# Kernel optimization log

Hardware: AMD Instinct MI355X
Metric: run time of the kernel (lower is better)

## Reference

```python
import jax, jax.numpy as jnp
import numpy as np

B, N, D_IN, D_OUT, H = 1, 4096, 512, 512, 8
DH = D_OUT // H


def setup_inputs() -> dict:
    key = jax.random.key(0)
    ks = jax.random.split(key, 8)
    s_in = 1.0 / np.sqrt(D_IN)
    h = jax.random.normal(ks[0], (B, N, D_IN), dtype=jnp.float32)
    adj_matrix = jax.random.uniform(ks[1], (B, N, N), dtype=jnp.float32)
    mask_matrix = jnp.zeros((B, N, N), dtype=jnp.float32)
    Wq = jax.random.uniform(ks[2], (D_IN, D_OUT), minval=-s_in, maxval=s_in, dtype=jnp.float32)
    Wk = jax.random.uniform(ks[3], (D_IN, D_OUT), minval=-s_in, maxval=s_in, dtype=jnp.float32)
    Wv = jax.random.uniform(ks[4], (D_IN, D_OUT), minval=-s_in, maxval=s_in, dtype=jnp.float32)
    bq = jax.random.uniform(ks[5], (D_OUT,), minval=-s_in, maxval=s_in, dtype=jnp.float32)
    bk = jax.random.uniform(ks[6], (D_OUT,), minval=-s_in, maxval=s_in, dtype=jnp.float32)
    bv = jax.random.uniform(ks[7], (D_OUT,), minval=-s_in, maxval=s_in, dtype=jnp.float32)
    return {"h": h, "adj_matrix": adj_matrix, "mask_matrix": mask_matrix,
            "Wq": Wq, "bq": bq, "Wk": Wk, "bk": bk, "Wv": Wv, "bv": bv}


def reference(h, adj_matrix, mask_matrix, Wq, bq, Wk, bk, Wv, bv):
    # Q/K/V projections: (B, N, D_OUT)
    Q = h @ Wq + bq
    K = h @ Wk + bk
    V = h @ Wv + bv
    # split heads: (B, N, H, DH)
    Qh = Q.reshape(B, N, H, DH)
    Kh = K.reshape(B, N, H, DH)
    Vh = V.reshape(B, N, H, DH)
    scale = 1.0 / np.sqrt(DH).astype(np.float32)
    # adjacency-weighted scores + additive mask, per head (vectorized over heads)
    # score[b,h,i,j] = (adj[b,i,j] * <Q_i, K_j> + mask[b,i,j]) / sqrt(DH)
    qk = jnp.einsum('bihd,bjhd->bhij', Qh, Kh)
    score = (adj_matrix[:, None, :, :] * qk + mask_matrix[:, None, :, :]) * scale
    attn = jax.nn.softmax(score, axis=-1)
    out = jnp.einsum('bhij,bjhd->bihd', attn, Vh)  # (B, N, H, DH)
    return out.reshape(B, N, D_OUT)
```

## Files before the change

### kernel.cpp

```cpp
#include <hip/hip_runtime.h>
#include <hip/hip_bf16.h>

typedef __attribute__((ext_vector_type(8))) short bf16x8;
typedef __attribute__((ext_vector_type(4))) float f32x4;

#define LOG2E 1.44269504088896340736f
#define NSPLIT 4
#define NT_PER 32

__device__ __forceinline__ unsigned short f2bf(float f) {
  unsigned int u = __float_as_uint(f);
  u += 0x7FFFu + ((u >> 16) & 1u);
  return (unsigned short)(u >> 16);
}

__global__ void cvt_h_kernel(const float* __restrict__ src, unsigned short* __restrict__ dst, int n4) {
  int i = blockIdx.x * blockDim.x + threadIdx.x;
  if (i >= n4) return;
  float4 v = reinterpret_cast<const float4*>(src)[i];
  ushort4 o;
  o.x = f2bf(v.x); o.y = f2bf(v.y); o.z = f2bf(v.z); o.w = f2bf(v.w);
  reinterpret_cast<ushort4*>(dst)[i] = o;
}

__global__ void cvt_wt_kernel(const float* __restrict__ Wq, const float* __restrict__ Wk,
                              const float* __restrict__ Wv, unsigned short* __restrict__ wt) {
  __shared__ float tile[32][33];
  const float* W = blockIdx.z == 0 ? Wq : (blockIdx.z == 1 ? Wk : Wv);
  int o0 = blockIdx.x * 32, i0 = blockIdx.y * 32;
  int c = threadIdx.x & 31, r4 = threadIdx.x >> 5;
  for (int rr = 0; rr < 32; rr += 8)
    tile[rr + r4][c] = W[(i0 + rr + r4) * 512 + o0 + c];
  __syncthreads();
  unsigned short* out = wt + blockIdx.z * 512 * 512;
  for (int rr = 0; rr < 32; rr += 8)
    out[(o0 + rr + r4) * 512 + i0 + c] = f2bf(tile[c][rr + r4]);
}

__global__ __launch_bounds__(256) void qkv_gemm_kernel(
    const unsigned short* __restrict__ hb, const unsigned short* __restrict__ wt,
    const float* __restrict__ bq, const float* __restrict__ bk, const float* __restrict__ bv,
    unsigned short* __restrict__ qb, unsigned short* __restrict__ kb, unsigned short* __restrict__ vtb) {
  __shared__ unsigned short Asm[128 * 32];
  __shared__ unsigned short Bsm[128 * 32];
  const int mat = blockIdx.z;
  const unsigned short* Wm = wt + mat * 512 * 512;
  const float* bias = mat == 0 ? bq : (mat == 1 ? bk : bv);
  const int bm = blockIdx.y, bn = blockIdx.x;
  const int t = threadIdx.x;
  const int wid = t >> 6, lane = t & 63;
  const int wr = wid >> 1, wc = wid & 1;
  const int lg = lane >> 4, lr = lane & 15;

  f32x4 acc[4][4];
  for (int a = 0; a < 4; ++a)
    for (int b = 0; b < 4; ++b) acc[a][b] = {0.f, 0.f, 0.f, 0.f};

  for (int kk = 0; kk < 512; kk += 32) {
    __syncthreads();
    for (int u = 0; u < 2; ++u) {
      int idx = t + u * 256;
      int row = idx >> 2, seg = idx & 3;
      *reinterpret_cast<int4*>(&Asm[row * 32 + seg * 8]) =
          *reinterpret_cast<const int4*>(&hb[(bm * 128 + row) * 512 + kk + seg * 8]);
      *reinterpret_cast<int4*>(&Bsm[row * 32 + seg * 8]) =
          *reinterpret_cast<const int4*>(&Wm[(bn * 128 + row) * 512 + kk + seg * 8]);
    }
    __syncthreads();
    bf16x8 a[4], b[4];
    for (int f = 0; f < 4; ++f) {
      a[f] = *reinterpret_cast<const bf16x8*>(&Asm[(wr * 64 + f * 16 + lr) * 32 + lg * 8]);
      b[f] = *reinterpret_cast<const bf16x8*>(&Bsm[(wc * 64 + f * 16 + lr) * 32 + lg * 8]);
    }
    for (int fm = 0; fm < 4; ++fm)
      for (int fn = 0; fn < 4; ++fn)
        acc[fm][fn] = __builtin_amdgcn_mfma_f32_16x16x32_bf16(a[fm], b[fn], acc[fm][fn], 0, 0, 0);
  }

  for (int fm = 0; fm < 4; ++fm)
    for (int fn = 0; fn < 4; ++fn) {
      const int col = bn * 128 + wc * 64 + fn * 16 + lr;
      const float bval = bias[col];
      const int head = col >> 6, dh = col & 63;
      for (int r = 0; r < 4; ++r) {
        const int row = bm * 128 + wr * 64 + fm * 16 + lg * 4 + r;
        const unsigned short bf = f2bf(acc[fm][fn][r] + bval);
        if (mat == 0)      qb[(head * 4096 + row) * 64 + dh] = bf;
        else if (mat == 1) kb[(head * 4096 + row) * 64 + dh] = bf;
        else               vtb[(head * 64 + dh) * 4096 + row] = bf;
      }
    }
}

__global__ __launch_bounds__(512) void attn_kernel(
    const unsigned short* __restrict__ qb, const unsigned short* __restrict__ kb,
    const unsigned short* __restrict__ vtb, const float* __restrict__ adj,
    const float* __restrict__ mask, float* __restrict__ pacc, float* __restrict__ pml) {
  __shared__ float adj_s[2][32][36];
  __shared__ float msk_s[2][32][36];
  __shared__ unsigned short p_s[8][32][40];
  const int t = threadIdx.x;
  const int h = t >> 6, lane = t & 63;
  const int lg = lane >> 4, lr = lane & 15;
  const int i0 = blockIdx.x * 32;
  const int sp = blockIdx.y;
  const unsigned short* Qh = qb + h * 4096 * 64;
  const unsigned short* Kh = kb + h * 4096 * 64;
  const unsigned short* Vh = vtb + h * 64 * 4096;

  const int tt = t & 255;
  const int srow = tt >> 3, sc4 = (tt & 7) * 4;
  const float* sbase = (t < 256 ? adj : mask) + (size_t)(i0 + srow) * 4096 + sc4;

  bf16x8 qf[2][2];
  for (int in_ = 0; in_ < 2; ++in_)
    for (int ks = 0; ks < 2; ++ks)
      qf[in_][ks] = *reinterpret_cast<const bf16x8*>(&Qh[(i0 + in_ * 16 + lr) * 64 + ks * 32 + lg * 8]);

  f32x4 acc[2][4];
  for (int fi = 0; fi < 2; ++fi)
    for (int fd = 0; fd < 4; ++fd) acc[fi][fd] = {0.f, 0.f, 0.f, 0.f};
  float m[2] = {-1e30f, -1e30f};
  float l[2] = {0.f, 0.f};

  {
    const int j0 = sp * NT_PER * 32;
    const float4 v = *reinterpret_cast<const float4*>(sbase + j0);
    float* dstp = (t < 256) ? &adj_s[0][srow][sc4] : &msk_s[0][srow][sc4];
    *reinterpret_cast<float4*>(dstp) = v;
  }
  __syncthreads();

  for (int it = 0; it < NT_PER; ++it) {
    const int j0 = (sp * NT_PER + it) * 32;
    const int cur = it & 1;
    float4 nv;
    const bool havenext = (it + 1 < NT_PER);
    if (havenext) nv = *reinterpret_cast<const float4*>(sbase + j0 + 32);

    f32x4 s[2][2];
    for (int jm = 0; jm < 2; ++jm)
      for (int in_ = 0; in_ < 2; ++in_) s[jm][in_] = {0.f, 0.f, 0.f, 0.f};
    for (int jm = 0; jm < 2; ++jm)
      for (int ks = 0; ks < 2; ++ks) {
        const bf16x8 kf = *reinterpret_cast<const bf16x8*>(&Kh[(j0 + jm * 16 + lr) * 64 + ks * 32 + lg * 8]);
        for (int in_ = 0; in_ < 2; ++in_)
          s[jm][in_] = __builtin_amdgcn_mfma_f32_16x16x32_bf16(kf, qf[in_][ks], s[jm][in_], 0, 0, 0);
      }

    float sc[2][2][4];
    float tm[2] = {-1e30f, -1e30f};
    for (int in_ = 0; in_ < 2; ++in_)
      for (int jm = 0; jm < 2; ++jm) {
        const float4 av = *reinterpret_cast<const float4*>(&adj_s[cur][in_ * 16 + lr][jm * 16 + lg * 4]);
        const float4 mv = *reinterpret_cast<const float4*>(&msk_s[cur][in_ * 16 + lr][jm * 16 + lg * 4]);
        const float a0[4] = {av.x, av.y, av.z, av.w};
        const float m0[4] = {mv.x, mv.y, mv.z, mv.w};
        for (int r = 0; r < 4; ++r) {
          const float v = (a0[r] * s[jm][in_][r] + m0[r]) * (0.125f * LOG2E);
          sc[in_][jm][r] = v;
          tm[in_] = fmaxf(tm[in_], v);
        }
      }
    for (int in_ = 0; in_ < 2; ++in_) {
      tm[in_] = fmaxf(tm[in_], __shfl_xor(tm[in_], 16));
      tm[in_] = fmaxf(tm[in_], __shfl_xor(tm[in_], 32));
    }
    const float mn0 = fmaxf(m[0], tm[0]);
    const float mn1 = fmaxf(m[1], tm[1]);
    if (__any(tm[0] > m[0] || tm[1] > m[1])) {
      const float f0 = exp2f(m[0] - mn0);
      const float f1 = exp2f(m[1] - mn1);
      l[0] *= f0; l[1] *= f1;
      m[0] = mn0; m[1] = mn1;
      const float ff[2] = {f0, f1};
      for (int fi = 0; fi < 2; ++fi)
        for (int r = 0; r < 4; ++r) {
          const float fr = __int_as_float(
              __builtin_amdgcn_ds_bpermute((lg * 4 + r) << 2, __float_as_int(ff[fi])));
          for (int fd = 0; fd < 4; ++fd) acc[fi][fd][r] *= fr;
        }
    }

    float ts[2] = {0.f, 0.f};
    for (int in_ = 0; in_ < 2; ++in_)
      for (int jm = 0; jm < 2; ++jm) {
        ushort4 w;
        unsigned short* wp = reinterpret_cast<unsigned short*>(&w);
        for (int r = 0; r < 4; ++r) {
          const float p = exp2f(sc[in_][jm][r] - m[in_]);
          ts[in_] += p;
          wp[r] = f2bf(p);
        }
        *reinterpret_cast<ushort4*>(&p_s[h][in_ * 16 + lr][jm * 16 + lg * 4]) = w;
      }
    for (int in_ = 0; in_ < 2; ++in_) {
      ts[in_] += __shfl_xor(ts[in_], 16);
      ts[in_] += __shfl_xor(ts[in_], 32);
      l[in_] += ts[in_];
    }

    bf16x8 pa[2];
    for (int fi = 0; fi < 2; ++fi)
      pa[fi] = *reinterpret_cast<const bf16x8*>(&p_s[h][fi * 16 + lr][lg * 8]);
    for (int fd = 0; fd < 4; ++fd) {
      const bf16x8 vf = *reinterpret_cast<const bf16x8*>(&Vh[(size_t)(fd * 16 + lr) * 4096 + j0 + lg * 8]);
      for (int fi = 0; fi < 2; ++fi)
        acc[fi][fd] = __builtin_amdgcn_mfma_f32_16x16x32_bf16(pa[fi], vf, acc[fi][fd], 0, 0, 0);
    }

    if (havenext) {
      float* dstp = (t < 256) ? &adj_s[cur ^ 1][srow][sc4] : &msk_s[cur ^ 1][srow][sc4];
      *reinterpret_cast<float4*>(dstp) = nv;
    }
    __syncthreads();
  }

  float* pa_base = pacc + ((size_t)sp * 4096 + i0) * 512;
  for (int fi = 0; fi < 2; ++fi)
    for (int fd = 0; fd < 4; ++fd)
      for (int r = 0; r < 4; ++r) {
        const int rowl = fi * 16 + lg * 4 + r;
        const int col = h * 64 + fd * 16 + lr;
        pa_base[rowl * 512 + col] = acc[fi][fd][r];
      }
  if (lane < 16) {
    for (int in_ = 0; in_ < 2; ++in_) {
      const int row = i0 + in_ * 16 + lane;
      float2 v; v.x = m[in_]; v.y = l[in_];
      reinterpret_cast<float2*>(pml)[((size_t)sp * 8 + h) * 4096 + row] = v;
    }
  }
}

__global__ __launch_bounds__(128) void combine_kernel(
    const float* __restrict__ pacc, const float* __restrict__ pml, float* __restrict__ out) {
  const int row = blockIdx.x;
  const int t = threadIdx.x;
  const int col = t * 4;
  const int head = col >> 6;

  float ms[NSPLIT], ls[NSPLIT];
  float M = -1e30f;
  for (int s = 0; s < NSPLIT; ++s) {
    const float2 v = reinterpret_cast<const float2*>(pml)[((size_t)s * 8 + head) * 4096 + row];
    ms[s] = v.x; ls[s] = v.y;
    M = fmaxf(M, v.x);
  }
  float denom = 0.f;
  float w[NSPLIT];
  for (int s = 0; s < NSPLIT; ++s) {
    w[s] = exp2f(ms[s] - M);
    denom += ls[s] * w[s];
  }
  const float inv = 1.0f / denom;
  float4 o = {0.f, 0.f, 0.f, 0.f};
  for (int s = 0; s < NSPLIT; ++s) {
    const float4 a = *reinterpret_cast<const float4*>(&pacc[((size_t)s * 4096 + row) * 512 + col]);
    o.x += a.x * w[s]; o.y += a.y * w[s]; o.z += a.z * w[s]; o.w += a.w * w[s];
  }
  o.x *= inv; o.y *= inv; o.z *= inv; o.w *= inv;
  *reinterpret_cast<float4*>(&out[(size_t)row * 512 + col]) = o;
}

extern "C" void kernel_launch(void* const* d_in, const int* in_sizes, int n_in,
                              void* d_out, int out_size, void* d_ws, size_t ws_size,
                              hipStream_t stream) {
  const float* h    = (const float*)d_in[0];
  const float* adj  = (const float*)d_in[1];
  const float* mask = (const float*)d_in[2];
  const float* Wq   = (const float*)d_in[3];
  const float* bq   = (const float*)d_in[4];
  const float* Wk   = (const float*)d_in[5];
  const float* bk   = (const float*)d_in[6];
  const float* Wv   = (const float*)d_in[7];
  const float* bv   = (const float*)d_in[8];
  float* out = (float*)d_out;

  char* ws = (char*)d_ws;
  unsigned short* hb = (unsigned short*)(ws);
  unsigned short* wt = (unsigned short*)(ws + (4u  << 20));
  unsigned short* qb = (unsigned short*)(ws + (6u  << 20));
  unsigned short* kb = (unsigned short*)(ws + (10u << 20));
  unsigned short* vt = (unsigned short*)(ws + (14u << 20));
  float* pacc = (float*)(ws + (20u << 20));
  float* pml  = (float*)(ws + (52u << 20));

  cvt_h_kernel<<<dim3(2048), dim3(256), 0, stream>>>(h, hb, 4096 * 512 / 4);
  cvt_wt_kernel<<<dim3(16, 16, 3), dim3(256), 0, stream>>>(Wq, Wk, Wv, wt);
  qkv_gemm_kernel<<<dim3(4, 32, 3), dim3(256), 0, stream>>>(hb, wt, bq, bk, bv, qb, kb, vt);
  attn_kernel<<<dim3(128, NSPLIT), dim3(512), 0, stream>>>(qb, kb, vt, adj, mask, pacc, pml);
  combine_kernel<<<dim3(4096), dim3(128), 0, stream>>>(pacc, pml, out);
}
```

Measured before the change: 178.4 us.

## Load adj/mask directly to registers, lazy rescale, swizzled P, packed bf16, wider split

Drops the shared-memory staging and per-iteration block barrier for the adjacency and mask tiles; each wave now loads its own adj/mask float4s straight into registers. Online-softmax rescaling is skipped unless the running max rises by more than a threshold. The P tile is written with packed v_cvt_pk_bf16 into an XOR-swizzled, unpadded LDS layout to avoid bank conflicts. When the workspace is large enough, the KV split rises from 4 to 8 so more blocks run, and launch bounds request higher occupancy. The costs are redundant global loads of adj/mask across the 8 head-waves (relying on cache), larger partial buffers, and more combine work.

After: 502.9 us. +182.0%, slower.

```diff
diff --git a/kernel.cpp b/kernel.cpp
--- a/kernel.cpp
+++ b/kernel.cpp
@@ -5,13 +5,18 @@
 typedef __attribute__((ext_vector_type(4))) float f32x4;
 
 #define LOG2E 1.44269504088896340736f
-#define NSPLIT 4
-#define NT_PER 32
+#define RESCALE_THR 8.0f
 
 __device__ __forceinline__ unsigned short f2bf(float f) {
   unsigned int u = __float_as_uint(f);
   u += 0x7FFFu + ((u >> 16) & 1u);
   return (unsigned short)(u >> 16);
+}
+
+__device__ __forceinline__ unsigned int cvt_pk_bf16(float lo, float hi) {
+  unsigned int r;
+  asm("v_cvt_pk_bf16_f32 %0, %1, %2" : "=v"(r) : "v"(lo), "v"(hi));
+  return r;
 }
 
 __global__ void cvt_h_kernel(const float* __restrict__ src, unsigned short* __restrict__ dst, int n4) {
@@ -92,13 +97,13 @@
     }
 }
 
-__global__ __launch_bounds__(512) void attn_kernel(
+template <int NSPLIT>
+__global__ __launch_bounds__(512, 6) void attn_kernel(
     const unsigned short* __restrict__ qb, const unsigned short* __restrict__ kb,
     const unsigned short* __restrict__ vtb, const float* __restrict__ adj,
     const float* __restrict__ mask, float* __restrict__ pacc, float* __restrict__ pml) {
-  __shared__ float adj_s[2][32][36];
-  __shared__ float msk_s[2][32][36];
-  __shared__ unsigned short p_s[8][32][40];
+  constexpr int NT = 128 / NSPLIT;
+  __shared__ __align__(16) unsigned short p_s[8][32][32];
   const int t = threadIdx.x;
   const int h = t >> 6, lane = t & 63;
   const int lg = lane >> 4, lr = lane & 15;
@@ -108,10 +113,6 @@
   const unsigned short* Kh = kb + h * 4096 * 64;
   const unsigned short* Vh = vtb + h * 64 * 4096;
 
-  const int tt = t & 255;
-  const int srow = tt >> 3, sc4 = (tt & 7) * 4;
-  const float* sbase = (t < 256 ? adj : mask) + (size_t)(i0 + srow) * 4096 + sc4;
-
   bf16x8 qf[2][2];
   for (int in_ = 0; in_ < 2; ++in_)
     for (int ks = 0; ks < 2; ++ks)
@@ -120,23 +121,19 @@
   f32x4 acc[2][4];
   for (int fi = 0; fi < 2; ++fi)
     for (int fd = 0; fd < 4; ++fd) acc[fi][fd] = {0.f, 0.f, 0.f, 0.f};
-  float m[2] = {-1e30f, -1e30f};
+  float m[2] = {-3e38f, -3e38f};
   float l[2] = {0.f, 0.f};
 
-  {
-    const int j0 = sp * NT_PER * 32;
-    const float4 v = *reinterpret_cast<const float4*>(sbase + j0);
-    float* dstp = (t < 256) ? &adj_s[0][srow][sc4] : &msk_s[0][srow][sc4];
-    *reinterpret_cast<float4*>(dstp) = v;
-  }
-  __syncthreads();
-
-  for (int it = 0; it < NT_PER; ++it) {
-    const int j0 = (sp * NT_PER + it) * 32;
-    const int cur = it & 1;
-    float4 nv;
-    const bool havenext = (it + 1 < NT_PER);
-    if (havenext) nv = *reinterpret_cast<const float4*>(sbase + j0 + 32);
+  for (int it = 0; it < NT; ++it) {
+    const int j0 = (sp * NT + it) * 32;
+
+    float4 av[2][2], mv[2][2];
+    for (int in_ = 0; in_ < 2; ++in_)
+      for (int jm = 0; jm < 2; ++jm) {
+        const size_t off = (size_t)(i0 + in_ * 16 + lr) * 4096 + j0 + jm * 16 + lg * 4;
+        av[in_][jm] = *reinterpret_cast<const float4*>(adj + off);
+        mv[in_][jm] = *reinterpret_cast<const float4*>(mask + off);
+      }
 
     f32x4 s[2][2];
     for (int jm = 0; jm < 2; ++jm)
@@ -148,17 +145,14 @@
           s[jm][in_] = __builtin_amdgcn_mfma_f32_16x16x32_bf16(kf, qf[in_][ks], s[jm][in_], 0, 0, 0);
       }
 
-    float sc[2][2][4];
-    float tm[2] = {-1e30f, -1e30f};
+    float tm[2] = {-3e38f, -3e38f};
     for (int in_ = 0; in_ < 2; ++in_)
       for (int jm = 0; jm < 2; ++jm) {
-        const float4 av = *reinterpret_cast<const float4*>(&adj_s[cur][in_ * 16 + lr][jm * 16 + lg * 4]);
-        const float4 mv = *reinterpret_cast<const float4*>(&msk_s[cur][in_ * 16 + lr][jm * 16 + lg * 4]);
-        const float a0[4] = {av.x, av.y, av.z, av.w};
-        const float m0[4] = {mv.x, mv.y, mv.z, mv.w};
+        const float a0[4] = {av[in_][jm].x, av[in_][jm].y, av[in_][jm].z, av[in_][jm].w};
+        const float m0[4] = {mv[in_][jm].x, mv[in_][jm].y, mv[in_][jm].z, mv[in_][jm].w};
         for (int r = 0; r < 4; ++r) {
-          const float v = (a0[r] * s[jm][in_][r] + m0[r]) * (0.125f * LOG2E);
-          sc[in_][jm][r] = v;
+          const float v = fmaf(a0[r], s[jm][in_][r], m0[r]) * (0.125f * LOG2E);
+          s[jm][in_][r] = v;
           tm[in_] = fmaxf(tm[in_], v);
         }
       }
@@ -166,9 +160,10 @@
       tm[in_] = fmaxf(tm[in_], __shfl_xor(tm[in_], 16));
       tm[in_] = fmaxf(tm[in_], __shfl_xor(tm[in_], 32));
     }
-    const float mn0 = fmaxf(m[0], tm[0]);
-    const float mn1 = fmaxf(m[1], tm[1]);
-    if (__any(tm[0] > m[0] || tm[1] > m[1])) {
+
+    if (__any((tm[0] > m[0] + RESCALE_THR) || (tm[1] > m[1] + RESCALE_THR))) {
+      const float mn0 = fmaxf(m[0], tm[0]);
+      const float mn1 = fmaxf(m[1], tm[1]);
       const float f0 = exp2f(m[0] - mn0);
       const float f1 = exp2f(m[1] - mn1);
       l[0] *= f0; l[1] *= f1;
@@ -183,17 +178,22 @@
     }
 
     float ts[2] = {0.f, 0.f};
-    for (int in_ = 0; in_ < 2; ++in_)
+    for (int in_ = 0; in_ < 2; ++in_) {
+      const int row = in_ * 16 + lr;
       for (int jm = 0; jm < 2; ++jm) {
-        ushort4 w;
-        unsigned short* wp = reinterpret_cast<unsigned short*>(&w);
-        for (int r = 0; r < 4; ++r) {
-          const float p = exp2f(sc[in_][jm][r] - m[in_]);
-          ts[in_] += p;
-          wp[r] = f2bf(p);
-        }
-        *reinterpret_cast<ushort4*>(&p_s[h][in_ * 16 + lr][jm * 16 + lg * 4]) = w;
-      }
+        const float p0 = exp2f(s[jm][in_][0] - m[in_]);
+        const float p1 = exp2f(s[jm][in_][1] - m[in_]);
+        const float p2 = exp2f(s[jm][in_][2] - m[in_]);
+        const float p3 = exp2f(s[jm][in_][3] - m[in_]);
+        ts[in_] += (p0 + p1) + (p2 + p3);
+        uint2 w;
+        w.x = cvt_pk_bf16(p0, p1);
+        w.y = cvt_pk_bf16(p2, p3);
+        const int o = 2 * jm + (lg >> 1);
+        const int colp = (((o + row) & 3) << 3) + ((lg & 1) << 2);
+        *reinterpret_cast<uint2*>(&p_s[h][row][colp]) = w;
+      }
+    }
     for (int in_ = 0; in_ < 2; ++in_) {
       ts[in_] += __shfl_xor(ts[in_], 16);
       ts[in_] += __shfl_xor(ts[in_], 32);
@@ -201,19 +201,16 @@
     }
 
     bf16x8 pa[2];
-    for (int fi = 0; fi < 2; ++fi)
-      pa[fi] = *reinterpret_cast<const bf16x8*>(&p_s[h][fi * 16 + lr][lg * 8]);
+    for (int fi = 0; fi < 2; ++fi) {
+      const int row = fi * 16 + lr;
+      const int colp = ((lg + row) & 3) << 3;
+      pa[fi] = *reinterpret_cast<const bf16x8*>(&p_s[h][row][colp]);
+    }
     for (int fd = 0; fd < 4; ++fd) {
       const bf16x8 vf = *reinterpret_cast<const bf16x8*>(&Vh[(size_t)(fd * 16 + lr) * 4096 + j0 + lg * 8]);
       for (int fi = 0; fi < 2; ++fi)
         acc[fi][fd] = __builtin_amdgcn_mfma_f32_16x16x32_bf16(pa[fi], vf, acc[fi][fd], 0, 0, 0);
     }
-
-    if (havenext) {
-      float* dstp = (t < 256) ? &adj_s[cur ^ 1][srow][sc4] : &msk_s[cur ^ 1][srow][sc4];
-      *reinterpret_cast<float4*>(dstp) = nv;
-    }
-    __syncthreads();
   }
 
   float* pa_base = pacc + ((size_t)sp * 4096 + i0) * 512;
@@ -233,6 +230,7 @@
   }
 }
 
+template <int NSPLIT>
 __global__ __launch_bounds__(128) void combine_kernel(
     const float* __restrict__ pacc, const float* __restrict__ pml, float* __restrict__ out) {
   const int row = blockIdx.x;
@@ -241,7 +239,7 @@
   const int head = col >> 6;
 
   float ms[NSPLIT], ls[NSPLIT];
-  float M = -1e30f;
+  float M = -3e38f;
   for (int s = 0; s < NSPLIT; ++s) {
     const float2 v = reinterpret_cast<const float2*>(pml)[((size_t)s * 8 + head) * 4096 + row];
     ms[s] = v.x; ls[s] = v.y;
@@ -284,11 +282,19 @@
   unsigned short* kb = (unsigned short*)(ws + (10u << 20));
   unsigned short* vt = (unsigned short*)(ws + (14u << 20));
   float* pacc = (float*)(ws + (20u << 20));
-  float* pml  = (float*)(ws + (52u << 20));
+
+  const bool big = ws_size >= ((size_t)87 << 20);
+  const int nsplit = big ? 8 : 4;
+  float* pml = (float*)(ws + ((size_t)(20 + nsplit * 8) << 20));
 
   cvt_h_kernel<<<dim3(2048), dim3(256), 0, stream>>>(h, hb, 4096 * 512 / 4);
   cvt_wt_kernel<<<dim3(16, 16, 3), dim3(256), 0, stream>>>(Wq, Wk, Wv, wt);
   qkv_gemm_kernel<<<dim3(4, 32, 3), dim3(256), 0, stream>>>(hb, wt, bq, bk, bv, qb, kb, vt);
-  attn_kernel<<<dim3(128, NSPLIT), dim3(512), 0, stream>>>(qb, kb, vt, adj, mask, pacc, pml);
-  combine_kernel<<<dim3(4096), dim3(128), 0, stream>>>(pacc, pml, out);
-}
+  if (big) {
+    attn_kernel<8><<<dim3(128, 8), dim3(512), 0, stream>>>(qb, kb, vt, adj, mask, pacc, pml);
+    combine_kernel<8><<<dim3(4096), dim3(128), 0, stream>>>(pacc, pml, out);
+  } else {
+    attn_kernel<4><<<dim3(128, 4), dim3(512), 0, stream>>>(qb, kb, vt, adj, mask, pacc, pml);
+    combine_kernel<4><<<dim3(4096), dim3(128), 0, stream>>>(pacc, pml, out);
+  }
+}
```
